# Performance work log

Hardware: AMD Instinct MI355X
Metric: run time of the kernel (lower is better)

## Reference

```python
import jax, jax.numpy as jnp
import numpy as np
from jax import lax

N = 20          # PARAM.N discretization steps
STEP_SIZE = 1.0 / N  # max_T / N = 1 / 20
B = 1_048_576   # number of Monte-Carlo paths


def _lin_init(key, fan_in, fan_out):
    kw, kb = jax.random.split(key)
    s = 1.0 / np.sqrt(fan_in)
    W = jax.random.uniform(kw, (fan_in, fan_out), minval=-s, maxval=s, dtype=jnp.float32)
    b = jax.random.uniform(kb, (fan_out,), minval=-s, maxval=s, dtype=jnp.float32)
    return W, b


def setup_inputs() -> dict:
    key = jax.random.key(0)
    ks = jax.random.split(key, 10)
    S0 = jax.random.uniform(ks[0], (B,), minval=50.0, maxval=150.0, dtype=jnp.float32)
    K = jax.random.uniform(ks[1], (B,), minval=50.0, maxval=150.0, dtype=jnp.float32)
    # maturities in {0.5, 1.0} per PARAM.maturities
    T = jnp.where(jax.random.bernoulli(ks[2], 0.5, (B,)), 0.5, 1.0).astype(jnp.float32)
    BM = jax.random.normal(ks[3], (B, N), dtype=jnp.float32)
    # 3 stacks: (4->30->5), (5->30->5), (5->30->2)
    W1, b1 = _lin_init(ks[4], 4, 30)
    W2, b2 = _lin_init(ks[5], 30, 5)
    W3, b3 = _lin_init(ks[6], 5, 30)
    W4, b4 = _lin_init(ks[7], 30, 5)
    W5, b5 = _lin_init(ks[8], 5, 30)
    W6, b6 = _lin_init(ks[9], 30, 2)
    return dict(S0=S0, K=K, T=T, BM=BM,
                W1=W1, b1=b1, W2=W2, b2=b2, W3=W3, b3=b3,
                W4=W4, b4=b4, W5=W5, b5=b5, W6=W6, b6=b6)


def reference(S0, K, T, BM, W1, b1, W2, b2, W3, b3, W4, b4, W5, b5, W6, b6):
    def net(x):  # [B,4] -> [B,2]
        h = jax.nn.relu(x @ W1 + b1) @ W2 + b2
        h = jax.nn.relu(h @ W3 + b3) @ W4 + b4
        return jax.nn.relu(h @ W5 + b5) @ W6 + b6

    def feats(price, time):  # [B,4] features: price, time, T-time, log(price/K)
        t = time * jnp.ones_like(price)
        return jnp.stack([price, t, T - t, jnp.log(price / K)], axis=-1)

    def step(carry, inp):
        price, hedgepf = carry
        idx, dW = inp
        time = (idx + 1.0) / N
        do_comp = (time <= T).astype(price.dtype)
        inc = dW * STEP_SIZE
        lev = net(feats(price, time))[:, 0]
        price = price + do_comp * lev * price * inc
        hed = net(feats(price, time))[:, 1] * inc
        hedgepf = hedgepf + do_comp * hed
        return (price, hedgepf), None

    init = (S0, jnp.zeros_like(S0))
    xs = (jnp.arange(N, dtype=S0.dtype), BM.T)  # scan over time steps
    (price, hedgepf), _ = lax.scan(step, init, xs)
    payoff = (price - K + jnp.abs(price - K)) * 0.5  # == relu(price - K)
    return payoff - hedgepf
```

## Files before the change

### kernel.cpp

```cpp
#include <hip/hip_runtime.h>

#define NSTEPS 20

typedef short bf16x8 __attribute__((ext_vector_type(8)));
typedef float f32x16 __attribute__((ext_vector_type(16)));

union B8 { bf16x8 h; unsigned u[4]; unsigned short s[8]; };

__device__ __forceinline__ unsigned short f2bf(float x) {
    unsigned u = __builtin_bit_cast(unsigned, x);
    u += 0x7fffu + ((u >> 16) & 1u);
    return (unsigned short)(u >> 16);
}
__device__ __forceinline__ float bf2f(unsigned short b) {
    return __builtin_bit_cast(float, (unsigned)b << 16);
}
__device__ __forceinline__ unsigned pk(unsigned short lo, unsigned short hi) {
    return (unsigned)lo | ((unsigned)hi << 16);
}
__device__ __forceinline__ unsigned cvtpk(float a, float b) {
    unsigned r;
    asm("v_cvt_pk_bf16_f32 %0, %1, %2" : "=v"(r) : "v"(a), "v"(b));
    return r;
}
__device__ __forceinline__ float lo_f(unsigned w) { return __builtin_bit_cast(float, w << 16); }
__device__ __forceinline__ float hi_f(unsigned w) { return __builtin_bit_cast(float, w & 0xffff0000u); }

#define MFMA(A, B, C) __builtin_amdgcn_mfma_f32_32x32x16_bf16((A), (B), (C), 0, 0, 0)
#define PRIO1() __builtin_amdgcn_s_setprio(1)
#define PRIO0() __builtin_amdgcn_s_setprio(0)

__device__ __forceinline__ void wlimbs(float w, unsigned short& l0, unsigned short& l1, unsigned short& l2) {
    l0 = f2bf(w); float e = w - bf2f(l0);
    l1 = f2bf(e); e -= bf2f(l1);
    l2 = f2bf(e);
}
__device__ __forceinline__ unsigned short pick(int m, unsigned short l0, unsigned short l1, unsigned short l2) {
    return (m == 0) ? l0 : ((m == 1) ? l1 : l2);
}


template<int F_, int M>
__device__ __forceinline__ bf16x8 awide(const float* W, const float* bias, int nout, int ld, int lane)
{
    const int u = lane & 31, h = (lane >> 5) & 1;
    B8 r;
#pragma unroll
    for (int j = 0; j < 8; ++j) {
        const int k = 16 * F_ + 4 * h + (j & 3) + 8 * (j >> 2);
        float v = 0.f;
        if (u < nout) {
            if (k < 30) v = W[k * ld + u];
            else if (k == 30) v = bias[u];
        }
        unsigned short l0, l1, l2; wlimbs(v, l0, l1, l2);
        r.s[j] = (short)pick(M, l0, l1, l2);
    }
    return r.h;
}

template<int S, int F_>
__device__ __forceinline__ bf16x8 a5(const float* W, const float* bias, int lane)
{
    const int u = lane & 31, h = (lane >> 5) & 1;
    B8 r;
#pragma unroll
    for (int j = 0; j < 8; ++j) {
        const int k = 16 * F_ + 4 * h + (j & 3) + 8 * (j >> 2);
        unsigned short bits = 0;
        if (u < 30) {
            int in = -1, m = -1;
            if (F_ == 0) {
                if (k < 4)       { in = k; m = S; }
                else if (k == 4) { in = 4; m = S; }
            } else {
                if (k >= 16 && k < 20)      { in = k - 16; m = (S == 0) ? 1 : ((S == 1) ? 0 : -1); }
                else if (k == 20)           { in = 4;      m = (S == 0) ? 1 : ((S == 1) ? 0 : -1); }
                else if (k >= 24 && k < 28) { in = k - 24; m = (S == 0) ? 2 : ((S == 2) ? 0 : -1); }
                else if (k == 21)           { in = 4;      m = (S == 0) ? 2 : ((S == 2) ? 0 : -1); }
            }
            if (in >= 0 && m >= 0) {
                unsigned short l0, l1, l2; wlimbs(W[in * 30 + u], l0, l1, l2);
                bits = pick(m, l0, l1, l2);
            } else if (F_ == 0 && k == 15) {
                unsigned short l0, l1, l2; wlimbs(bias[u], l0, l1, l2);
                bits = pick(S, l0, l1, l2);
            }
        }
        r.s[j] = (short)bits;
    }
    return r.h;
}

template<int S>
__device__ __forceinline__ bf16x8 a1f(const float* W1, const float* b1v, int lane)
{
    const int perm[4] = {0, 3, 1, 2};
    const int u = lane & 31, h = (lane >> 5) & 1;
    B8 r;
#pragma unroll
    for (int j = 0; j < 8; ++j) {
        const int k = 4 * h + (j & 3) + 8 * (j >> 2);
        unsigned short bits = 0;
        if (u < 30) {
            int in = -1, m = -1;
            if (k < 4)       { in = k;     m = (S == 0) ? 0 : ((S == 1) ? 1 : 2); }
            else if (k < 8)  { in = k - 4; m = (S == 0) ? 1 : ((S == 1) ? 0 : -1); }
            else if (k < 12) { in = k - 8; m = (S == 0) ? 2 : ((S == 2) ? 0 : -1); }
            if (in >= 0 && m >= 0) {
                unsigned short l0, l1, l2; wlimbs(W1[perm[in] * 30 + u], l0, l1, l2);
                bits = pick(m, l0, l1, l2);
            } else if (k == 12) {
                unsigned short l0, l1, l2; wlimbs(b1v[u], l0, l1, l2);
                bits = pick(S, l0, l1, l2);
            }
        }
        r.s[j] = (short)bits;
    }
    return r.h;
}


template<int LIMBS>
__device__ __forceinline__ void split_pair(float a, float b,
                                           unsigned& w0, unsigned& w1, unsigned& w2)
{
    w0 = cvtpk(a, b);
    if (LIMBS >= 2) {
        float e0 = a - lo_f(w0), e1 = b - hi_f(w0);
        w1 = cvtpk(e0, e1);
        if (LIMBS == 3) {
            float f0 = e0 - lo_f(w1), f1 = e1 - hi_f(w1);
            w2 = cvtpk(f0, f1);
        } else w2 = 0u;
    } else { w1 = 0u; w2 = 0u; }
}

template<int LIMBS>
__device__ __forceinline__ void split30(const f32x16& acc, bool hi,
                                        B8& B0a, B8& B0b, B8& B1a, B8& B1b,
                                        B8& B2a, B8& B2b)
{
#pragma unroll
    for (int i = 0; i < 4; ++i) {
        const float a = fmaxf(acc[2 * i], 0.f), b = fmaxf(acc[2 * i + 1], 0.f);
        unsigned w0, w1, w2; split_pair<LIMBS>(a, b, w0, w1, w2);
        B0a.u[i] = w0;
        if (LIMBS >= 2) B1a.u[i] = w1;
        if (LIMBS == 3) B2a.u[i] = w2;
    }
#pragma unroll
    for (int i = 0; i < 4; ++i) {
        const float a = fmaxf(acc[8 + 2 * i], 0.f), b = fmaxf(acc[8 + 2 * i + 1], 0.f);
        unsigned w0, w1, w2; split_pair<LIMBS>(a, b, w0, w1, w2);
        B0b.u[i] = w0;
        if (LIMBS >= 2) B1b.u[i] = w1;
        if (LIMBS == 3) B2b.u[i] = w2;
    }
    if (hi) {
        B0b.u[3] = 0x00003F80u;
        if (LIMBS >= 2) B1b.u[3] = 0u;
        if (LIMBS == 3) B2b.u[3] = 0u;
    }
}

template<int LIMBS>
__device__ __forceinline__ void split5(const f32x16& acc, bool hi, B8& C0, B8& C1)
{
    const float a0 = acc[0], a1 = acc[1];
    const float a2 = acc[2], a3 = acc[3];
    unsigned p0, p1, p2, q0, q1, q2;
    split_pair<LIMBS>(a0, a1, p0, p1, p2);
    split_pair<LIMBS>(a2, a3, q0, q1, q2);
    if (!hi) {
        C0.u[0] = p0; C0.u[1] = q0; C0.u[2] = 0; C0.u[3] = 0;
        if (LIMBS >= 2) {
            C1.u[0] = p1; C1.u[1] = q1;
            C1.u[2] = (LIMBS == 3) ? p2 : 0u;
            C1.u[3] = (LIMBS == 3) ? q2 : 0u;
        }
    } else {
        C0.u[0] = p0 & 0xffffu;
        C0.u[1] = 0; C0.u[2] = 0;
        C0.u[3] = 0x3F800000u;
        if (LIMBS >= 2) {
            C1.u[0] = (LIMBS == 3) ? pk((unsigned short)(p1 & 0xffffu), (unsigned short)(p2 & 0xffffu))
                                   : (p1 & 0xffffu);
            C1.u[1] = 0; C1.u[2] = 0; C1.u[3] = 0;
        }
    }
}

#define NFRAG 27

template<int LIMBS>
__device__ __forceinline__ f32x16 evalnet5(
    float price, float f3, unsigned tT0, unsigned tT1, unsigned tT2,
    bool hi, const bf16x8* LF, int lane, const f32x16& Z)
{
    unsigned pf0, pf1, pf2;
    split_pair<LIMBS>(price, f3, pf0, pf1, pf2);
    B8 B;
    if (!hi) {
        B.u[0] = pf0; B.u[1] = tT0;
        B.u[2] = (LIMBS == 3) ? pf2 : 0u;
        B.u[3] = (LIMBS == 3) ? tT2 : 0u;
    } else {
        B.u[0] = (LIMBS >= 2) ? pf1 : 0u;
        B.u[1] = (LIMBS >= 2) ? tT1 : 0u;
        B.u[2] = 0x00003F80u;
        B.u[3] = 0u;
    }

    PRIO1();
    f32x16 acc = MFMA(LF[0 * 64 + lane], B.h, Z);
    if (LIMBS >= 2) acc = MFMA(LF[1 * 64 + lane], B.h, acc);
    if (LIMBS == 3) acc = MFMA(LF[2 * 64 + lane], B.h, acc);
    PRIO0();

    B8 B0a, B0b, B1a, B1b, B2a, B2b, C0, C1;
    f32x16 p, q;

    split30<LIMBS>(acc, hi, B0a, B0b, B1a, B1b, B2a, B2b);
    PRIO1();
    p = MFMA(LF[3 * 64 + lane], B0a.h, Z);
    q = MFMA(LF[4 * 64 + lane], B0b.h, Z);
    if (LIMBS >= 2) {
        p = MFMA(LF[3 * 64 + lane], B1a.h, p);
        q = MFMA(LF[4 * 64 + lane], B1b.h, q);
        if (LIMBS == 3) { p = MFMA(LF[3 * 64 + lane], B2a.h, p); q = MFMA(LF[4 * 64 + lane], B2b.h, q); }
        p = MFMA(LF[5 * 64 + lane], B0a.h, p);
        q = MFMA(LF[6 * 64 + lane], B0b.h, q);
        p = MFMA(LF[5 * 64 + lane], B1a.h, p);
        q = MFMA(LF[6 * 64 + lane], B1b.h, q);
        if (LIMBS == 3) { p = MFMA(LF[7 * 64 + lane], B0a.h, p); q = MFMA(LF[8 * 64 + lane], B0b.h, q); }
    }
    PRIO0();
    acc = p + q;

    split5<LIMBS>(acc, hi, C0, C1);
    PRIO1();
    if (LIMBS >= 2) {
        p = MFMA(LF[9 * 64 + lane], C0.h, Z);
        q = MFMA(LF[10 * 64 + lane], C1.h, Z);
        p = MFMA(LF[11 * 64 + lane], C0.h, p);
        q = MFMA(LF[12 * 64 + lane], C1.h, q);
        if (LIMBS == 3) { p = MFMA(LF[13 * 64 + lane], C0.h, p); q = MFMA(LF[14 * 64 + lane], C1.h, q); }
        acc = p + q;
    } else {
        acc = MFMA(LF[9 * 64 + lane], C0.h, Z);
    }
    PRIO0();

    split30<LIMBS>(acc, hi, B0a, B0b, B1a, B1b, B2a, B2b);
    PRIO1();
    p = MFMA(LF[15 * 64 + lane], B0a.h, Z);
    q = MFMA(LF[16 * 64 + lane], B0b.h, Z);
    if (LIMBS >= 2) {
        p = MFMA(LF[15 * 64 + lane], B1a.h, p);
        q = MFMA(LF[16 * 64 + lane], B1b.h, q);
        if (LIMBS == 3) { p = MFMA(LF[15 * 64 + lane], B2a.h, p); q = MFMA(LF[16 * 64 + lane], B2b.h, q); }
        p = MFMA(LF[17 * 64 + lane], B0a.h, p);
        q = MFMA(LF[18 * 64 + lane], B0b.h, q);
        p = MFMA(LF[17 * 64 + lane], B1a.h, p);
        q = MFMA(LF[18 * 64 + lane], B1b.h, q);
        if (LIMBS == 3) { p = MFMA(LF[19 * 64 + lane], B0a.h, p); q = MFMA(LF[20 * 64 + lane], B0b.h, q); }
    }
    PRIO0();
    acc = p + q;

    split5<LIMBS>(acc, hi, C0, C1);
    PRIO1();
    if (LIMBS >= 2) {
        p = MFMA(LF[21 * 64 + lane], C0.h, Z);
        q = MFMA(LF[22 * 64 + lane], C1.h, Z);
        p = MFMA(LF[23 * 64 + lane], C0.h, p);
        q = MFMA(LF[24 * 64 + lane], C1.h, q);
        if (LIMBS == 3) { p = MFMA(LF[25 * 64 + lane], C0.h, p); q = MFMA(LF[26 * 64 + lane], C1.h, q); }
        acc = p + q;
    } else {
        acc = MFMA(LF[21 * 64 + lane], C0.h, Z);
    }
    PRIO0();

    return acc;
}

template<int COL>
__device__ __forceinline__ float l6dot(const f32x16& a5v, bool hi, const float* __restrict__ W6)
{
    float part = 0.f;
    if (!hi) {
#pragma unroll
        for (int r = 0; r < 16; ++r) {
            const int row = (r & 3) + 8 * (r >> 2);
            part = fmaf(fmaxf(a5v[r], 0.f), W6[row * 2 + COL], part);
        }
    } else {
#pragma unroll
        for (int r = 0; r < 16; ++r) {
            const int row = (r & 3) + 8 * (r >> 2) + 4;
            if (row < 30) part = fmaf(fmaxf(a5v[r], 0.f), W6[row * 2 + COL], part);
        }
    }
    part += __shfl_xor(part, 32);
    return part;
}

__global__ __launch_bounds__(1024) void partition_kernel(
    const float* __restrict__ Tv, int* __restrict__ ws, int Btot)
{
    __shared__ int cntA[16], cntB[16], baseSh[2];
    const int tid = threadIdx.x;
    const int wid = tid >> 6;
    const int lane = tid & 63;
    const int i = blockIdx.x * 1024 + tid;
    const bool valid = i < Btot;
    const bool isLong  = valid && (Tv[valid ? i : 0] > 0.75f);
    const bool isShort = valid && !isLong;
    const unsigned long long mA = __ballot(isLong);
    const unsigned long long mB = __ballot(isShort);
    const unsigned long long ltm = (1ull << lane) - 1ull;

    if (lane == 0) { cntA[wid] = __popcll(mA); cntB[wid] = __popcll(mB); }
    __syncthreads();
    if (tid == 0) {
        int ta = 0, tb = 0;
#pragma unroll
        for (int k = 0; k < 16; ++k) {
            const int a = cntA[k]; cntA[k] = ta; ta += a;
            const int b = cntB[k]; cntB[k] = tb; tb += b;
        }
        baseSh[0] = ta ? atomicAdd(&ws[0], ta) : 0;
        baseSh[1] = tb ? atomicAdd(&ws[1], tb) : 0;
    }
    __syncthreads();

    int* list = ws + 16;
    if (isLong) {
        const int pos = baseSh[0] + cntA[wid] + __popcll(mA & ltm);
        list[pos] = i;
    }
    if (isShort) {
        const int pos = baseSh[1] + cntB[wid] + __popcll(mB & ltm);
        list[Btot - 1 - pos] = i;
    }
}

template<int LIST>
__global__ __launch_bounds__(256) __attribute__((amdgpu_waves_per_eu(4, 8)))
void mc_hedge_mfma(
    const float* __restrict__ S0, const float* __restrict__ Kv,
    const float* __restrict__ Tv, const float* __restrict__ BM,
    const float* __restrict__ W1, const float* __restrict__ b1,
    const float* __restrict__ W2, const float* __restrict__ b2,
    const float* __restrict__ W3, const float* __restrict__ b3,
    const float* __restrict__ W4, const float* __restrict__ b4,
    const float* __restrict__ W5, const float* __restrict__ b5,
    const float* __restrict__ W6, const float* __restrict__ b6,
    const int* __restrict__ list, float* __restrict__ out, int Btot)
{
    __shared__ bf16x8 LFs[NFRAG * 64];

    const int lane = threadIdx.x & 63;
    const int wid  = threadIdx.x >> 6;

    if (wid == 0) {
        LFs[0 * 64 + lane]  = a1f<0>(W1, b1, lane);
        LFs[1 * 64 + lane]  = a1f<1>(W1, b1, lane);
        LFs[2 * 64 + lane]  = a1f<2>(W1, b1, lane);
        LFs[3 * 64 + lane]  = awide<0,0>(W2, b2, 5, 5, lane);
        LFs[4 * 64 + lane]  = awide<1,0>(W2, b2, 5, 5, lane);
        LFs[5 * 64 + lane]  = awide<0,1>(W2, b2, 5, 5, lane);
        LFs[6 * 64 + lane]  = awide<1,1>(W2, b2, 5, 5, lane);
        LFs[7 * 64 + lane]  = awide<0,2>(W2, b2, 5, 5, lane);
        LFs[8 * 64 + lane]  = awide<1,2>(W2, b2, 5, 5, lane);
        LFs[9 * 64 + lane]  = a5<0,0>(W3, b3, lane);
        LFs[10 * 64 + lane] = a5<0,1>(W3, b3, lane);
        LFs[11 * 64 + lane] = a5<1,0>(W3, b3, lane);
        LFs[12 * 64 + lane] = a5<1,1>(W3, b3, lane);
        LFs[13 * 64 + lane] = a5<2,0>(W3, b3, lane);
        LFs[14 * 64 + lane] = a5<2,1>(W3, b3, lane);
        LFs[15 * 64 + lane] = awide<0,0>(W4, b4, 5, 5, lane);
        LFs[16 * 64 + lane] = awide<1,0>(W4, b4, 5, 5, lane);
        LFs[17 * 64 + lane] = awide<0,1>(W4, b4, 5, 5, lane);
        LFs[18 * 64 + lane] = awide<1,1>(W4, b4, 5, 5, lane);
        LFs[19 * 64 + lane] = awide<0,2>(W4, b4, 5, 5, lane);
        LFs[20 * 64 + lane] = awide<1,2>(W4, b4, 5, 5, lane);
        LFs[21 * 64 + lane] = a5<0,0>(W5, b5, lane);
        LFs[22 * 64 + lane] = a5<0,1>(W5, b5, lane);
        LFs[23 * 64 + lane] = a5<1,0>(W5, b5, lane);
        LFs[24 * 64 + lane] = a5<1,1>(W5, b5, lane);
        LFs[25 * 64 + lane] = a5<2,0>(W5, b5, lane);
        LFs[26 * 64 + lane] = a5<2,1>(W5, b5, lane);
    }
    __syncthreads();
    const bf16x8* LF = LFs;

    const int base = blockIdx.x * 128 + wid * 32;
    if (base >= Btot) return;
    const int li = min(base + (lane & 31), Btot - 1);
    const int p = LIST ? list[li] : li;
    const bool hi = lane >= 32;

    const float b60 = b6[0], b61 = b6[1];

    f32x16 Z;
#pragma unroll
    for (int i = 0; i < 16; ++i) Z[i] = 0.0f;

    float price = S0[p];
    const float Kk = Kv[p];
    const float T  = Tv[p];
    const float logK = __logf(Kk);
    float hedge = 0.0f;
    const float* bmrow = BM + (size_t)p * NSTEPS;

    int wsteps = NSTEPS;
    if (LIST) {
        const int st = (T > 0.75f) ? NSTEPS : (NSTEPS / 2);
        wsteps = __shfl(st, 0);
    }

#pragma unroll 1
    for (int idx = 0; idx < wsteps; ++idx) {
        const float time = (float)(idx + 1) / (float)NSTEPS;
        const float docomp = (time <= T) ? 1.0f : 0.0f;
        const float inc = bmrow[idx] * (1.0f / (float)NSTEPS);
        const float tmt = T - time;

        unsigned tT0, tT1, tT2;
        split_pair<3>(time, tmt, tT0, tT1, tT2);

        float f3 = __logf(price) - logK;
        f32x16 a5v = evalnet5<3>(price, f3, tT0, tT1, tT2, hi, LF, lane, Z);
        const float lev = l6dot<0>(a5v, hi, W6) + b60;
        price = price + docomp * lev * price * inc;

        f3 = __logf(price) - logK;
        a5v = evalnet5<1>(price, f3, tT0, tT1, tT2, hi, LF, lane, Z);
        const float hed = (l6dot<1>(a5v, hi, W6) + b61) * inc;
        hedge = hedge + docomp * hed;
    }

    if (!hi && (base + lane) < Btot) {
        const float payoff = fmaxf(price - Kk, 0.0f);
        out[p] = payoff - hedge;
    }
}

extern "C" void kernel_launch(void* const* d_in, const int* in_sizes, int n_in,
                              void* d_out, int out_size, void* d_ws, size_t ws_size,
                              hipStream_t stream)
{
    const float* S0 = (const float*)d_in[0];
    const float* Kv = (const float*)d_in[1];
    const float* Tv = (const float*)d_in[2];
    const float* BM = (const float*)d_in[3];
    const float* W1 = (const float*)d_in[4];
    const float* b1 = (const float*)d_in[5];
    const float* W2 = (const float*)d_in[6];
    const float* b2 = (const float*)d_in[7];
    const float* W3 = (const float*)d_in[8];
    const float* b3 = (const float*)d_in[9];
    const float* W4 = (const float*)d_in[10];
    const float* b4 = (const float*)d_in[11];
    const float* W5 = (const float*)d_in[12];
    const float* b5 = (const float*)d_in[13];
    const float* W6 = (const float*)d_in[14];
    const float* b6 = (const float*)d_in[15];

    float* out = (float*)d_out;
    const int B = in_sizes[0];
    const int gridC = (B + 127) / 128;
    const size_t need = (size_t)(16 + B) * sizeof(int);

    if (ws_size >= need) {
        int* ws = (int*)d_ws;
        hipMemsetAsync(ws, 0, 16 * sizeof(int), stream);
        partition_kernel<<<(B + 1023) / 1024, 1024, 0, stream>>>(Tv, ws, B);
        mc_hedge_mfma<1><<<gridC, 256, 0, stream>>>(
            S0, Kv, Tv, BM, W1, b1, W2, b2, W3, b3, W4, b4, W5, b5, W6, b6,
            ws + 16, out, B);
    } else {
        mc_hedge_mfma<0><<<gridC, 256, 0, stream>>>(
            S0, Kv, Tv, BM, W1, b1, W2, b2, W3, b3, W4, b4, W5, b5, W6, b6,
            (const int*)nullptr, out, B);
    }
}
```

Before: 703.9 us.

## Fuse hedge eval of step t with leverage eval of step t+1

Restructures the time loop so the hedge network at step t and the leverage network at step t+1 use the same price and are evaluated together in one interleaved MFMA chain. It peels a leverage-only prologue and a hedge-only epilogue. The two independent dependency chains are meant to hide MFMA latency and share the split work. The occupancy hint is also lowered so the fused path can use more registers, at the cost of fewer resident waves.

New measurement: 711.5 us. Within noise of the previous version (+1.1%).

```diff
diff --git a/kernel.cpp b/kernel.cpp
--- a/kernel.cpp
+++ b/kernel.cpp
@@ -286,6 +286,104 @@
     return acc;
 }
 
+__device__ __forceinline__ void evalnet_fused(
+    unsigned pf0, unsigned pf1, unsigned pf2, unsigned th0,
+    unsigned tl0, unsigned tl1, unsigned tl2,
+    bool hi, const bf16x8* LF, int lane, const f32x16& Z,
+    f32x16& outH, f32x16& outL)
+{
+    B8 Bh, Bl;
+    if (!hi) {
+        Bh.u[0] = pf0; Bh.u[1] = th0; Bh.u[2] = 0u;          Bh.u[3] = 0u;
+        Bl.u[0] = pf0; Bl.u[1] = tl0; Bl.u[2] = pf2;         Bl.u[3] = tl2;
+    } else {
+        Bh.u[0] = 0u;  Bh.u[1] = 0u;  Bh.u[2] = 0x00003F80u; Bh.u[3] = 0u;
+        Bl.u[0] = pf1; Bl.u[1] = tl1; Bl.u[2] = 0x00003F80u; Bl.u[3] = 0u;
+    }
+
+    PRIO1();
+    f32x16 ah = MFMA(LF[0 * 64 + lane], Bh.h, Z);
+    f32x16 al = MFMA(LF[0 * 64 + lane], Bl.h, Z);
+    al = MFMA(LF[1 * 64 + lane], Bl.h, al);
+    al = MFMA(LF[2 * 64 + lane], Bl.h, al);
+    PRIO0();
+
+    B8 H0a, H0b, Hd1, Hd2, Hd3, Hd4, Hc0, Hc1;
+    B8 L0a, L0b, L1a, L1b, L2a, L2b, Lc0, Lc1;
+    f32x16 p, q, ph, qh;
+
+    split30<1>(ah, hi, H0a, H0b, Hd1, Hd2, Hd3, Hd4);
+    split30<3>(al, hi, L0a, L0b, L1a, L1b, L2a, L2b);
+    PRIO1();
+    ph = MFMA(LF[3 * 64 + lane], H0a.h, Z);
+    qh = MFMA(LF[4 * 64 + lane], H0b.h, Z);
+    p = MFMA(LF[3 * 64 + lane], L0a.h, Z);
+    q = MFMA(LF[4 * 64 + lane], L0b.h, Z);
+    p = MFMA(LF[3 * 64 + lane], L1a.h, p);
+    q = MFMA(LF[4 * 64 + lane], L1b.h, q);
+    p = MFMA(LF[3 * 64 + lane], L2a.h, p);
+    q = MFMA(LF[4 * 64 + lane], L2b.h, q);
+    p = MFMA(LF[5 * 64 + lane], L0a.h, p);
+    q = MFMA(LF[6 * 64 + lane], L0b.h, q);
+    p = MFMA(LF[5 * 64 + lane], L1a.h, p);
+    q = MFMA(LF[6 * 64 + lane], L1b.h, q);
+    p = MFMA(LF[7 * 64 + lane], L0a.h, p);
+    q = MFMA(LF[8 * 64 + lane], L0b.h, q);
+    PRIO0();
+    ah = ph + qh;
+    al = p + q;
+
+    split5<1>(ah, hi, Hc0, Hc1);
+    split5<3>(al, hi, Lc0, Lc1);
+    PRIO1();
+    ah = MFMA(LF[9 * 64 + lane], Hc0.h, Z);
+    p = MFMA(LF[9 * 64 + lane], Lc0.h, Z);
+    q = MFMA(LF[10 * 64 + lane], Lc1.h, Z);
+    p = MFMA(LF[11 * 64 + lane], Lc0.h, p);
+    q = MFMA(LF[12 * 64 + lane], Lc1.h, q);
+    p = MFMA(LF[13 * 64 + lane], Lc0.h, p);
+    q = MFMA(LF[14 * 64 + lane], Lc1.h, q);
+    PRIO0();
+    al = p + q;
+
+    split30<1>(ah, hi, H0a, H0b, Hd1, Hd2, Hd3, Hd4);
+    split30<3>(al, hi, L0a, L0b, L1a, L1b, L2a, L2b);
+    PRIO1();
+    ph = MFMA(LF[15 * 64 + lane], H0a.h, Z);
+    qh = MFMA(LF[16 * 64 + lane], H0b.h, Z);
+    p = MFMA(LF[15 * 64 + lane], L0a.h, Z);
+    q = MFMA(LF[16 * 64 + lane], L0b.h, Z);
+    p = MFMA(LF[15 * 64 + lane], L1a.h, p);
+    q = MFMA(LF[16 * 64 + lane], L1b.h, q);
+    p = MFMA(LF[15 * 64 + lane], L2a.h, p);
+    q = MFMA(LF[16 * 64 + lane], L2b.h, q);
+    p = MFMA(LF[17 * 64 + lane], L0a.h, p);
+    q = MFMA(LF[18 * 64 + lane], L0b.h, q);
+    p = MFMA(LF[17 * 64 + lane], L1a.h, p);
+    q = MFMA(LF[18 * 64 + lane], L1b.h, q);
+    p = MFMA(LF[19 * 64 + lane], L0a.h, p);
+    q = MFMA(LF[20 * 64 + lane], L0b.h, q);
+    PRIO0();
+    ah = ph + qh;
+    al = p + q;
+
+    split5<1>(ah, hi, Hc0, Hc1);
+    split5<3>(al, hi, Lc0, Lc1);
+    PRIO1();
+    ah = MFMA(LF[21 * 64 + lane], Hc0.h, Z);
+    p = MFMA(LF[21 * 64 + lane], Lc0.h, Z);
+    q = MFMA(LF[22 * 64 + lane], Lc1.h, Z);
+    p = MFMA(LF[23 * 64 + lane], Lc0.h, p);
+    q = MFMA(LF[24 * 64 + lane], Lc1.h, q);
+    p = MFMA(LF[25 * 64 + lane], Lc0.h, p);
+    q = MFMA(LF[26 * 64 + lane], Lc1.h, q);
+    PRIO0();
+    al = p + q;
+
+    outH = ah;
+    outL = al;
+}
+
 template<int COL>
 __device__ __forceinline__ float l6dot(const f32x16& a5v, bool hi, const float* __restrict__ W6)
 {
@@ -348,7 +446,7 @@
 }
 
 template<int LIST>
-__global__ __launch_bounds__(256) __attribute__((amdgpu_waves_per_eu(4, 8)))
+__global__ __launch_bounds__(256) __attribute__((amdgpu_waves_per_eu(3, 8)))
 void mc_hedge_mfma(
     const float* __restrict__ S0, const float* __restrict__ Kv,
     const float* __restrict__ Tv, const float* __restrict__ BM,
@@ -422,25 +520,58 @@
         wsteps = __shfl(st, 0);
     }
 
+    unsigned ct0, ct1, ct2;
+
+    {
+        const float time0 = (float)1 / (float)NSTEPS;
+        const float tmt0 = T - time0;
+        split_pair<3>(time0, tmt0, ct0, ct1, ct2);
+        const float dc0 = (time0 <= T) ? 1.0f : 0.0f;
+        const float inc0 = bmrow[0] * (1.0f / (float)NSTEPS);
+        float f3 = __logf(price) - logK;
+        f32x16 a = evalnet5<3>(price, f3, ct0, ct1, ct2, hi, LF, lane, Z);
+        const float lev = l6dot<0>(a, hi, W6) + b60;
+        price = price + dc0 * lev * price * inc0;
+    }
+
 #pragma unroll 1
-    for (int idx = 0; idx < wsteps; ++idx) {
-        const float time = (float)(idx + 1) / (float)NSTEPS;
-        const float docomp = (time <= T) ? 1.0f : 0.0f;
-        const float inc = bmrow[idx] * (1.0f / (float)NSTEPS);
-        const float tmt = T - time;
-
-        unsigned tT0, tT1, tT2;
-        split_pair<3>(time, tmt, tT0, tT1, tT2);
-
-        float f3 = __logf(price) - logK;
-        f32x16 a5v = evalnet5<3>(price, f3, tT0, tT1, tT2, hi, LF, lane, Z);
-        const float lev = l6dot<0>(a5v, hi, W6) + b60;
-        price = price + docomp * lev * price * inc;
-
-        f3 = __logf(price) - logK;
-        a5v = evalnet5<1>(price, f3, tT0, tT1, tT2, hi, LF, lane, Z);
-        const float hed = (l6dot<1>(a5v, hi, W6) + b61) * inc;
-        hedge = hedge + docomp * hed;
+    for (int idx = 0; idx < wsteps - 1; ++idx) {
+        const float timeH = (float)(idx + 1) / (float)NSTEPS;
+        const float timeL = (float)(idx + 2) / (float)NSTEPS;
+        const float dcH = (timeH <= T) ? 1.0f : 0.0f;
+        const float dcL = (timeL <= T) ? 1.0f : 0.0f;
+        const float incH = bmrow[idx] * (1.0f / (float)NSTEPS);
+        const float incL = bmrow[idx + 1] * (1.0f / (float)NSTEPS);
+        const float tmtL = T - timeL;
+
+        unsigned nl0, nl1, nl2;
+        split_pair<3>(timeL, tmtL, nl0, nl1, nl2);
+
+        const float f3 = __logf(price) - logK;
+        unsigned pf0, pf1, pf2;
+        split_pair<3>(price, f3, pf0, pf1, pf2);
+
+        f32x16 aH, aL;
+        evalnet_fused(pf0, pf1, pf2, ct0, nl0, nl1, nl2, hi, LF, lane, Z, aH, aL);
+
+        const float hed = (l6dot<1>(aH, hi, W6) + b61) * incH;
+        hedge = hedge + dcH * hed;
+
+        const float lev = l6dot<0>(aL, hi, W6) + b60;
+        price = price + dcL * lev * price * incL;
+
+        ct0 = nl0;
+    }
+
+    {
+        const int idx = wsteps - 1;
+        const float timeH = (float)(idx + 1) / (float)NSTEPS;
+        const float dcH = (timeH <= T) ? 1.0f : 0.0f;
+        const float incH = bmrow[idx] * (1.0f / (float)NSTEPS);
+        const float f3 = __logf(price) - logK;
+        f32x16 aH = evalnet5<1>(price, f3, ct0, 0u, 0u, hi, LF, lane, Z);
+        const float hed = (l6dot<1>(aH, hi, W6) + b61) * incH;
+        hedge = hedge + dcH * hed;
     }
 
     if (!hi && (base + lane) < Btot) {
```
